# Kernel tuning notes

Hardware: AMD Instinct MI355X
Metric: run time of the kernel (lower is better)

The kernel has to match this reference:

```python
import jax, jax.numpy as jnp
import numpy as np

N_NODES = 10000
N_EDGES = 640000
D = 128  # node / edge / hidden feature dim
EPS = 1e-6


def _relu_mlp(x, params):
    # Dense+relu for all layers except the last (plain Dense)
    for w, b in params[:-1]:
        x = jax.nn.relu(x @ w + b)
    w, b = params[-1]
    return x @ w + b


def _layer_norm(x, scale, bias):
    mean = jnp.mean(x, axis=-1, keepdims=True)
    var = jnp.mean(jnp.square(x - mean), axis=-1, keepdims=True)
    return (x - mean) * jax.lax.rsqrt(var + EPS) * scale + bias


def _he(key, fan_in, fan_out):
    return jax.random.normal(key, (fan_in, fan_out), jnp.float32) * jnp.sqrt(2.0 / fan_in)


def setup_inputs() -> dict:
    key = jax.random.key(0)
    ks = jax.random.split(key, 12)
    nodes = jax.random.normal(ks[0], (N_NODES, D), jnp.float32)
    edges = jax.random.normal(ks[1], (N_EDGES, D), jnp.float32)
    senders = jax.random.randint(ks[2], (N_EDGES,), 0, N_NODES, jnp.int32)
    receivers = jax.random.randint(ks[3], (N_EDGES,), 0, N_NODES, jnp.int32)
    # MessageMLP: [3D -> D -> D -> D]
    msg_w0 = _he(ks[4], 3 * D, D); msg_b0 = jnp.zeros((D,), jnp.float32)
    msg_w1 = _he(ks[5], D, D);     msg_b1 = jnp.zeros((D,), jnp.float32)
    msg_w2 = _he(ks[6], D, D);     msg_b2 = jnp.zeros((D,), jnp.float32)
    # NodeMLP: [2D -> D -> D -> D]
    node_w0 = _he(ks[7], 2 * D, D); node_b0 = jnp.zeros((D,), jnp.float32)
    node_w1 = _he(ks[8], D, D);     node_b1 = jnp.zeros((D,), jnp.float32)
    node_w2 = _he(ks[9], D, D);     node_b2 = jnp.zeros((D,), jnp.float32)
    # W_node residual projection (no bias) + LayerNorm params
    w_node = _he(ks[10], D, D)
    ln_scale = jnp.ones((D,), jnp.float32)
    ln_bias = jnp.zeros((D,), jnp.float32)
    return dict(nodes=nodes, edges=edges, senders=senders, receivers=receivers,
                msg_w0=msg_w0, msg_b0=msg_b0, msg_w1=msg_w1, msg_b1=msg_b1,
                msg_w2=msg_w2, msg_b2=msg_b2,
                node_w0=node_w0, node_b0=node_b0, node_w1=node_w1, node_b1=node_b1,
                node_w2=node_w2, node_b2=node_b2,
                w_node=w_node, ln_scale=ln_scale, ln_bias=ln_bias)


def reference(nodes, edges, senders, receivers,
              msg_w0, msg_b0, msg_w1, msg_b1, msg_w2, msg_b2,
              node_w0, node_b0, node_w1, node_b1, node_w2, node_b2,
              w_node, ln_scale, ln_bias):
    total_nodes = nodes.shape[0]
    # gather sender/receiver features and concat with edge features: [E, 3D]
    msg_in = jnp.concatenate([nodes[senders], nodes[receivers], edges], axis=-1)
    messages = _relu_mlp(msg_in, [(msg_w0, msg_b0), (msg_w1, msg_b1), (msg_w2, msg_b2)])
    # scatter-add messages onto receiving nodes: [N, D]
    aggregated = jax.ops.segment_sum(messages, receivers, num_segments=total_nodes)
    node_in = jnp.concatenate([nodes, aggregated], axis=-1)  # [N, 2D]
    nodes_out = _relu_mlp(node_in, [(node_w0, node_b0), (node_w1, node_b1), (node_w2, node_b2)])
    nodes_new = _layer_norm(nodes @ w_node + nodes_out, ln_scale, ln_bias)
    return nodes_new
```

## Files before the change

### kernel.cpp

```cpp
#include <hip/hip_runtime.h>

#define DF 128
constexpr int N_NODES = 10000;
constexpr int N_EDGES = 640000;

typedef __bf16 bf16x8 __attribute__((ext_vector_type(8)));
typedef float f32x4 __attribute__((ext_vector_type(4)));

__device__ __forceinline__ unsigned short f2bf(float f) {
  unsigned u = __builtin_bit_cast(unsigned, f);
  u += 0x7fffu + ((u >> 16) & 1u);
  return (unsigned short)(u >> 16);
}

__device__ __forceinline__ bf16x8 cvt8(float4 a, float4 b) {
  bf16x8 r;
  r[0] = (__bf16)a.x; r[1] = (__bf16)a.y; r[2] = (__bf16)a.z; r[3] = (__bf16)a.w;
  r[4] = (__bf16)b.x; r[5] = (__bf16)b.y; r[6] = (__bf16)b.z; r[7] = (__bf16)b.w;
  return r;
}

template <bool RELU>
__device__ __forceinline__ void stage_t(char* bufj, const f32x4* accv, int grp, int row16) {
#pragma unroll
  for (int nt = 0; nt < 8; ++nt)
#pragma unroll
    for (int i = 0; i < 4; ++i) {
      const int r = grp * 4 + i;
      const int c = nt * 16 + row16;
      float v = RELU ? fmaxf(accv[nt][i], 0.f) : accv[nt][i];
      *(unsigned short*)(bufj + ((r * 256 + c * 2) ^ ((r & 7) << 4))) = f2bf(v);
    }
}

__device__ __forceinline__ bf16x8 read_a(const char* bufj, int kt, int grp, int row16) {
  return *(const bf16x8*)(bufj + ((row16 * 256 + kt * 64 + grp * 16) ^ ((row16 & 7) << 4)));
}

__global__ void pack_prep(const float* __restrict__ w0, const float* __restrict__ w1,
                          const float* __restrict__ w2, const float* __restrict__ nw0,
                          const float* __restrict__ nw1, const float* __restrict__ nw2,
                          const float* __restrict__ wn, const float* __restrict__ nodes,
                          unsigned short* __restrict__ dst, unsigned short* __restrict__ nbf) {
  int tid = blockIdx.x * blockDim.x + threadIdx.x;
  if (tid >= 163840 + N_NODES * DF) return;
  if (tid >= 163840) {
    int p = tid - 163840;
    nbf[p] = f2bf(nodes[p]);
    return;
  }
  const float* src; int p;
  if (tid < 49152)       { src = w0;  p = tid; }
  else if (tid < 65536)  { src = w1;  p = tid - 49152; }
  else if (tid < 81920)  { src = w2;  p = tid - 65536; }
  else if (tid < 114688) { src = nw0; p = tid - 81920; }
  else if (tid < 131072) { src = nw1; p = tid - 114688; }
  else if (tid < 147456) { src = nw2; p = tid - 131072; }
  else                   { src = wn;  p = tid - 147456; }
  int i = p & 7, lane = (p >> 3) & 63, tile = p >> 9;
  int nt = tile & 7, kt = tile >> 3;
  int k = kt * 32 + ((lane >> 4) << 3) + i;
  int n = nt * 16 + (lane & 15);
  dst[tid] = f2bf(src[k * 128 + n]);
}

__global__ void hist_kernel(const int* __restrict__ receivers, int* __restrict__ deg) {
  int e = blockIdx.x * blockDim.x + threadIdx.x;
  if (e < N_EDGES) atomicAdd(&deg[receivers[e]], 1);
}

__global__ void scan_kernel(const int* __restrict__ deg, int* __restrict__ rowstart) {
  __shared__ int part[1024];
  const int t = threadIdx.x;
  int loc[16];
  int s = 0;
#pragma unroll
  for (int j = 0; j < 16; ++j) {
    int idx = t * 16 + j;
    int v = (idx < N_NODES) ? deg[idx] : 0;
    loc[j] = s;
    s += v;
  }
  part[t] = s;
  __syncthreads();
  for (int off = 1; off < 1024; off <<= 1) {
    int v = part[t];
    int a = (t >= off) ? part[t - off] : 0;
    __syncthreads();
    part[t] = v + a;
    __syncthreads();
  }
  int base = (t > 0) ? part[t - 1] : 0;
#pragma unroll
  for (int j = 0; j < 16; ++j) {
    int idx = t * 16 + j;
    if (idx < N_NODES) rowstart[idx] = base + loc[j];
  }
  if (t == 0) rowstart[N_NODES] = part[1023];
}

__global__ void scatter_idx(const int* __restrict__ receivers, const int* __restrict__ senders,
                            const int* __restrict__ rowstart,
                            int* __restrict__ cursor, int* __restrict__ eid,
                            int* __restrict__ rid, int* __restrict__ ssend) {
  int e = blockIdx.x * blockDim.x + threadIdx.x;
  if (e >= N_EDGES) return;
  int r = receivers[e];
  int pos = atomicAdd(&cursor[r], 1);
  int q = rowstart[r] + pos;
  eid[q] = e;
  rid[q] = r;
  ssend[q] = senders[e];
}

__global__ void __launch_bounds__(256) pq_kernel(
    const unsigned short* __restrict__ nbf, const unsigned short* __restrict__ pw,
    float* __restrict__ P, float* __restrict__ Q) {
  const int tid = threadIdx.x, lane = tid & 63, wave = tid >> 6;
  const int row16 = lane & 15, grp = lane >> 4;
  const int rb = blockIdx.x * 64 + wave * 16;
  const int rA = min(rb + row16, N_NODES - 1);

  f32x4 aP[8], aQ[8];
#pragma unroll
  for (int nt = 0; nt < 8; ++nt) {
    aP[nt] = (f32x4){0.f, 0.f, 0.f, 0.f};
    aQ[nt] = (f32x4){0.f, 0.f, 0.f, 0.f};
  }
#pragma unroll
  for (int kt = 0; kt < 4; ++kt) {
    bf16x8 af = *(const bf16x8*)(nbf + (size_t)rA * DF + kt * 32 + grp * 8);
#pragma unroll
    for (int nt = 0; nt < 8; ++nt) {
      bf16x8 bwP = *(const bf16x8*)(pw + ((size_t)(kt * 8 + nt) * 64 + lane) * 8);
      bf16x8 bwQ = *(const bf16x8*)(pw + ((size_t)((4 + kt) * 8 + nt) * 64 + lane) * 8);
      aP[nt] = __builtin_amdgcn_mfma_f32_16x16x32_bf16(af, bwP, aP[nt], 0, 0, 0);
      aQ[nt] = __builtin_amdgcn_mfma_f32_16x16x32_bf16(af, bwQ, aQ[nt], 0, 0, 0);
    }
  }
#pragma unroll
  for (int nt = 0; nt < 8; ++nt)
#pragma unroll
    for (int i = 0; i < 4; ++i) {
      const int r = rb + grp * 4 + i;
      if (r < N_NODES) {
        P[(size_t)r * DF + nt * 16 + row16] = aP[nt][i];
        Q[(size_t)r * DF + nt * 16 + row16] = aQ[nt][i];
      }
    }
}

__global__ void __launch_bounds__(256, 2) msg_kernel(
    const float* __restrict__ edges,
    const int* __restrict__ eid, const int* __restrict__ rid, const int* __restrict__ ssend,
    const float* __restrict__ b0, const float* __restrict__ b1,
    const unsigned short* __restrict__ pw,
    const float* __restrict__ P, const float* __restrict__ Q,
    float* __restrict__ hsum) {
  __shared__ char hs[65536];
  const int tid = threadIdx.x;
  const int lane = tid & 63, wave = tid >> 6;
  const int row16 = lane & 15, grp = lane >> 4;
  char* hb = hs + wave * 16384;
  const int pbase = blockIdx.x * 256 + wave * 64;

  int e_[4], rx[4], sx[4];
#pragma unroll
  for (int s = 0; s < 4; ++s) {
    const int p = pbase + s * 16 + row16;
    e_[s] = eid[p];
    rx[s] = rid[p];
    sx[s] = ssend[p];
  }

  bf16x8 ebf[4][4];
  {
    float4 t0[4][2], t1[4][2];
#pragma unroll
    for (int k2 = 0; k2 < 4; ++k2) {
      const float* p0 = edges + (size_t)e_[0] * DF + k2 * 32 + grp * 8;
      const float* p1 = edges + (size_t)e_[1] * DF + k2 * 32 + grp * 8;
      t0[k2][0] = *(const float4*)p0; t0[k2][1] = *(const float4*)(p0 + 4);
      t1[k2][0] = *(const float4*)p1; t1[k2][1] = *(const float4*)(p1 + 4);
    }
#pragma unroll
    for (int k2 = 0; k2 < 4; ++k2) {
      ebf[0][k2] = cvt8(t0[k2][0], t0[k2][1]);
      ebf[1][k2] = cvt8(t1[k2][0], t1[k2][1]);
    }
#pragma unroll
    for (int k2 = 0; k2 < 4; ++k2) {
      const float* p2 = edges + (size_t)e_[2] * DF + k2 * 32 + grp * 8;
      const float* p3 = edges + (size_t)e_[3] * DF + k2 * 32 + grp * 8;
      t0[k2][0] = *(const float4*)p2; t0[k2][1] = *(const float4*)(p2 + 4);
      t1[k2][0] = *(const float4*)p3; t1[k2][1] = *(const float4*)(p3 + 4);
    }
#pragma unroll
    for (int k2 = 0; k2 < 4; ++k2) {
      ebf[2][k2] = cvt8(t0[k2][0], t0[k2][1]);
      ebf[3][k2] = cvt8(t1[k2][0], t1[k2][1]);
    }
  }

  f32x4 acc[4][8];
#pragma unroll
  for (int nt = 0; nt < 8; ++nt) {
    float bv = b0[nt * 16 + row16];
#pragma unroll
    for (int s = 0; s < 4; ++s) acc[s][nt] = (f32x4){bv, bv, bv, bv};
  }
#pragma unroll
  for (int kt = 0; kt < 4; ++kt) {
#pragma unroll
    for (int nt = 0; nt < 8; ++nt) {
      bf16x8 bw = *(const bf16x8*)(pw + ((size_t)((8 + kt) * 8 + nt) * 64 + lane) * 8);
#pragma unroll
      for (int s = 0; s < 4; ++s)
        acc[s][nt] = __builtin_amdgcn_mfma_f32_16x16x32_bf16(ebf[s][kt], bw, acc[s][nt], 0, 0, 0);
    }
  }

#pragma unroll
  for (int s = 0; s < 4; ++s) stage_t<false>(hb + s * 4096, acc[s], grp, row16);
  asm volatile("s_waitcnt lgkmcnt(0)" ::: "memory");
  __builtin_amdgcn_sched_barrier(0);

  f32x4 acc2[4][8];
#pragma unroll
  for (int nt = 0; nt < 8; ++nt) {
    float bv = b1[nt * 16 + row16];
#pragma unroll
    for (int s = 0; s < 4; ++s) acc2[s][nt] = (f32x4){bv, bv, bv, bv};
  }
  const unsigned short* w1p = pw + 49152;
#pragma unroll
  for (int kt = 0; kt < 4; ++kt) {
    bf16x8 af[4];
#pragma unroll
    for (int s = 0; s < 4; ++s) {
      const float* pp = P + (size_t)sx[s] * DF + kt * 32 + grp * 8;
      const float* qq = Q + (size_t)rx[s] * DF + kt * 32 + grp * 8;
      float4 p0 = *(const float4*)pp, p1 = *(const float4*)(pp + 4);
      float4 q0 = *(const float4*)qq, q1 = *(const float4*)(qq + 4);
      bf16x8 raw = read_a(hb + s * 4096, kt, grp, row16);
      bf16x8 h;
      h[0] = (__bf16)fmaxf((float)raw[0] + p0.x + q0.x, 0.f);
      h[1] = (__bf16)fmaxf((float)raw[1] + p0.y + q0.y, 0.f);
      h[2] = (__bf16)fmaxf((float)raw[2] + p0.z + q0.z, 0.f);
      h[3] = (__bf16)fmaxf((float)raw[3] + p0.w + q0.w, 0.f);
      h[4] = (__bf16)fmaxf((float)raw[4] + p1.x + q1.x, 0.f);
      h[5] = (__bf16)fmaxf((float)raw[5] + p1.y + q1.y, 0.f);
      h[6] = (__bf16)fmaxf((float)raw[6] + p1.z + q1.z, 0.f);
      h[7] = (__bf16)fmaxf((float)raw[7] + p1.w + q1.w, 0.f);
      af[s] = h;
    }
#pragma unroll
    for (int nt = 0; nt < 8; ++nt) {
      bf16x8 bw = *(const bf16x8*)(w1p + ((size_t)(kt * 8 + nt) * 64 + lane) * 8);
#pragma unroll
      for (int s = 0; s < 4; ++s)
        acc2[s][nt] = __builtin_amdgcn_mfma_f32_16x16x32_bf16(af[s], bw, acc2[s][nt], 0, 0, 0);
    }
  }

#pragma unroll
  for (int s = 0; s < 4; ++s) {
    const int q = pbase + s * 16 + grp * 4;
    const int ru = rid[pbase + s * 16];
    const bool uni = (ru == rid[pbase + s * 16 + 15]);
    if (uni) {
#pragma unroll
      for (int nt = 0; nt < 8; ++nt) {
        float t = fmaxf(acc2[s][nt][0], 0.f) + fmaxf(acc2[s][nt][1], 0.f) +
                  fmaxf(acc2[s][nt][2], 0.f) + fmaxf(acc2[s][nt][3], 0.f);
        t += __shfl_xor(t, 16);
        t += __shfl_xor(t, 32);
        if (grp == 0)
          unsafeAtomicAdd(hsum + (size_t)ru * DF + nt * 16 + row16, t);
      }
    } else {
      const int ra = rid[q], rb_ = rid[q + 1], rc = rid[q + 2], rd = rid[q + 3];
#pragma unroll
      for (int nt = 0; nt < 8; ++nt) {
        const int col = nt * 16 + row16;
        float run = fmaxf(acc2[s][nt][0], 0.f);
        if (rb_ != ra) { unsafeAtomicAdd(hsum + (size_t)ra * DF + col, run); run = 0.f; }
        run += fmaxf(acc2[s][nt][1], 0.f);
        if (rc != rb_) { unsafeAtomicAdd(hsum + (size_t)rb_ * DF + col, run); run = 0.f; }
        run += fmaxf(acc2[s][nt][2], 0.f);
        if (rd != rc) { unsafeAtomicAdd(hsum + (size_t)rc * DF + col, run); run = 0.f; }
        run += fmaxf(acc2[s][nt][3], 0.f);
        unsafeAtomicAdd(hsum + (size_t)rd * DF + col, run);
      }
    }
  }
}

__global__ void __launch_bounds__(256) node_kernel(
    const float* __restrict__ nodes, const float* __restrict__ hsum,
    const int* __restrict__ deg, const float* __restrict__ b2,
    const float* __restrict__ nb0, const float* __restrict__ nb1, const float* __restrict__ nb2,
    const unsigned short* __restrict__ pw2,
    const unsigned short* __restrict__ pnw0, const unsigned short* __restrict__ pnw1,
    const unsigned short* __restrict__ pnw2, const unsigned short* __restrict__ pwn,
    const float* __restrict__ ln_s, const float* __restrict__ ln_b,
    float* __restrict__ out) {
  __shared__ char hs[16384];
  const int tid = threadIdx.x, lane = tid & 63, wave = tid >> 6;
  const int row16 = lane & 15, grp = lane >> 4;
  char* hb = hs + wave * 4096;
  const int rb = blockIdx.x * 64 + wave * 16;
  const int rA = min(rb + row16, N_NODES - 1);

  f32x4 accA[8];
  {
    float d0 = (float)deg[min(rb + grp * 4 + 0, N_NODES - 1)];
    float d1 = (float)deg[min(rb + grp * 4 + 1, N_NODES - 1)];
    float d2 = (float)deg[min(rb + grp * 4 + 2, N_NODES - 1)];
    float d3 = (float)deg[min(rb + grp * 4 + 3, N_NODES - 1)];
#pragma unroll
    for (int nt = 0; nt < 8; ++nt) {
      float bc = b2[nt * 16 + row16];
      accA[nt] = (f32x4){d0 * bc, d1 * bc, d2 * bc, d3 * bc};
    }
  }
#pragma unroll
  for (int kt = 0; kt < 4; ++kt) {
    const float* hp = hsum + (size_t)rA * DF + kt * 32 + grp * 8;
    float4 h0 = *(const float4*)hp, h1v = *(const float4*)(hp + 4);
    bf16x8 hi = cvt8(h0, h1v);
    float4 l0, l1;
    l0.x = h0.x - (float)hi[0]; l0.y = h0.y - (float)hi[1];
    l0.z = h0.z - (float)hi[2]; l0.w = h0.w - (float)hi[3];
    l1.x = h1v.x - (float)hi[4]; l1.y = h1v.y - (float)hi[5];
    l1.z = h1v.z - (float)hi[6]; l1.w = h1v.w - (float)hi[7];
    bf16x8 lo = cvt8(l0, l1);
#pragma unroll
    for (int nt = 0; nt < 8; ++nt) {
      bf16x8 bw = *(const bf16x8*)(pw2 + ((size_t)(kt * 8 + nt) * 64 + lane) * 8);
      accA[nt] = __builtin_amdgcn_mfma_f32_16x16x32_bf16(hi, bw, accA[nt], 0, 0, 0);
      accA[nt] = __builtin_amdgcn_mfma_f32_16x16x32_bf16(lo, bw, accA[nt], 0, 0, 0);
    }
  }
  stage_t<false>(hb, accA, grp, row16);
  asm volatile("s_waitcnt lgkmcnt(0)" ::: "memory");
  __builtin_amdgcn_sched_barrier(0);

  f32x4 acc[8];
#pragma unroll
  for (int nt = 0; nt < 8; ++nt) {
    float b = nb0[nt * 16 + row16];
    acc[nt] = (f32x4){b, b, b, b};
  }
#pragma unroll
  for (int kt = 0; kt < 8; ++kt) {
    bf16x8 af;
    if (kt < 4) {
      const float* p = nodes + (size_t)rA * DF + kt * 32 + grp * 8;
      af = cvt8(*(const float4*)p, *(const float4*)(p + 4));
    } else {
      af = read_a(hb, kt - 4, grp, row16);
    }
#pragma unroll
    for (int nt = 0; nt < 8; ++nt) {
      bf16x8 bw = *(const bf16x8*)(pnw0 + ((size_t)(kt * 8 + nt) * 64 + lane) * 8);
      acc[nt] = __builtin_amdgcn_mfma_f32_16x16x32_bf16(af, bw, acc[nt], 0, 0, 0);
    }
  }
  asm volatile("s_waitcnt lgkmcnt(0)" ::: "memory");
  __builtin_amdgcn_sched_barrier(0);
  stage_t<true>(hb, acc, grp, row16);
  asm volatile("s_waitcnt lgkmcnt(0)" ::: "memory");
  __builtin_amdgcn_sched_barrier(0);

  f32x4 acc2[8];
#pragma unroll
  for (int nt = 0; nt < 8; ++nt) {
    float b = nb1[nt * 16 + row16];
    acc2[nt] = (f32x4){b, b, b, b};
  }
#pragma unroll
  for (int kt = 0; kt < 4; ++kt) {
    bf16x8 af = read_a(hb, kt, grp, row16);
#pragma unroll
    for (int nt = 0; nt < 8; ++nt) {
      bf16x8 bw = *(const bf16x8*)(pnw1 + ((size_t)(kt * 8 + nt) * 64 + lane) * 8);
      acc2[nt] = __builtin_amdgcn_mfma_f32_16x16x32_bf16(af, bw, acc2[nt], 0, 0, 0);
    }
  }
  asm volatile("s_waitcnt lgkmcnt(0)" ::: "memory");
  __builtin_amdgcn_sched_barrier(0);
  stage_t<true>(hb, acc2, grp, row16);
  asm volatile("s_waitcnt lgkmcnt(0)" ::: "memory");
  __builtin_amdgcn_sched_barrier(0);

  f32x4 acc3[8];
#pragma unroll
  for (int nt = 0; nt < 8; ++nt) {
    float b = nb2[nt * 16 + row16];
    acc3[nt] = (f32x4){b, b, b, b};
  }
#pragma unroll
  for (int kt = 0; kt < 4; ++kt) {
    bf16x8 af = read_a(hb, kt, grp, row16);
#pragma unroll
    for (int nt = 0; nt < 8; ++nt) {
      bf16x8 bw = *(const bf16x8*)(pnw2 + ((size_t)(kt * 8 + nt) * 64 + lane) * 8);
      acc3[nt] = __builtin_amdgcn_mfma_f32_16x16x32_bf16(af, bw, acc3[nt], 0, 0, 0);
    }
  }
  f32x4 accR[8];
#pragma unroll
  for (int nt = 0; nt < 8; ++nt) accR[nt] = (f32x4){0.f, 0.f, 0.f, 0.f};
#pragma unroll
  for (int kt = 0; kt < 4; ++kt) {
    const float* p = nodes + (size_t)rA * DF + kt * 32 + grp * 8;
    bf16x8 af = cvt8(*(const float4*)p, *(const float4*)(p + 4));
#pragma unroll
    for (int nt = 0; nt < 8; ++nt) {
      bf16x8 bw = *(const bf16x8*)(pwn + ((size_t)(kt * 8 + nt) * 64 + lane) * 8);
      accR[nt] = __builtin_amdgcn_mfma_f32_16x16x32_bf16(af, bw, accR[nt], 0, 0, 0);
    }
  }

  float y[8][4];
#pragma unroll
  for (int nt = 0; nt < 8; ++nt)
#pragma unroll
    for (int i = 0; i < 4; ++i) y[nt][i] = acc3[nt][i] + accR[nt][i];

  float mean[4], rstd[4];
#pragma unroll
  for (int i = 0; i < 4; ++i) {
    float s = 0.f;
#pragma unroll
    for (int nt = 0; nt < 8; ++nt) s += y[nt][i];
    s += __shfl_xor(s, 1); s += __shfl_xor(s, 2);
    s += __shfl_xor(s, 4); s += __shfl_xor(s, 8);
    mean[i] = s * (1.0f / 128.0f);
  }
#pragma unroll
  for (int i = 0; i < 4; ++i) {
    float v = 0.f;
#pragma unroll
    for (int nt = 0; nt < 8; ++nt) {
      float d = y[nt][i] - mean[i];
      v += d * d;
    }
    v += __shfl_xor(v, 1); v += __shfl_xor(v, 2);
    v += __shfl_xor(v, 4); v += __shfl_xor(v, 8);
    rstd[i] = rsqrtf(v * (1.0f / 128.0f) + 1e-6f);
  }
#pragma unroll
  for (int nt = 0; nt < 8; ++nt) {
    const float ls = ln_s[nt * 16 + row16];
    const float lb = ln_b[nt * 16 + row16];
#pragma unroll
    for (int i = 0; i < 4; ++i) {
      const int r = rb + grp * 4 + i;
      if (r < N_NODES)
        out[(size_t)r * DF + nt * 16 + row16] = (y[nt][i] - mean[i]) * rstd[i] * ls + lb;
    }
  }
}

extern "C" void kernel_launch(void* const* d_in, const int* in_sizes, int n_in,
                              void* d_out, int out_size, void* d_ws, size_t ws_size,
                              hipStream_t stream) {
  const float* nodes     = (const float*)d_in[0];
  const float* edges     = (const float*)d_in[1];
  const int*   senders   = (const int*)d_in[2];
  const int*   receivers = (const int*)d_in[3];
  const float* msg_w0 = (const float*)d_in[4];
  const float* msg_b0 = (const float*)d_in[5];
  const float* msg_w1 = (const float*)d_in[6];
  const float* msg_b1 = (const float*)d_in[7];
  const float* msg_w2 = (const float*)d_in[8];
  const float* msg_b2 = (const float*)d_in[9];
  const float* node_w0 = (const float*)d_in[10];
  const float* node_b0 = (const float*)d_in[11];
  const float* node_w1 = (const float*)d_in[12];
  const float* node_b1 = (const float*)d_in[13];
  const float* node_w2 = (const float*)d_in[14];
  const float* node_b2 = (const float*)d_in[15];
  const float* w_node   = (const float*)d_in[16];
  const float* ln_scale = (const float*)d_in[17];
  const float* ln_bias  = (const float*)d_in[18];

  char* ws = (char*)d_ws;
  float* hsum           = (float*)ws;
  unsigned short* pw    = (unsigned short*)(ws + 5120000);
  unsigned short* nbf   = (unsigned short*)(ws + 5447680);
  int* deg              = (int*)(ws + 8007680);
  int* cursor           = (int*)(ws + 8047680);
  int* rowstart         = (int*)(ws + 8087680);
  int* eid              = (int*)(ws + 8127688);
  int* rid              = (int*)(ws + 10687688);
  int* ssend            = (int*)(ws + 13247688);
  float* P              = (float*)(ws + 15807744);
  float* Q              = (float*)(ws + 20927744);

  hipMemsetAsync(hsum, 0, (size_t)N_NODES * DF * sizeof(float), stream);
  hipMemsetAsync(deg, 0, 80000, stream);

  pack_prep<<<(163840 + N_NODES * DF) / 256, 256, 0, stream>>>(
      msg_w0, msg_w1, msg_w2, node_w0, node_w1, node_w2, w_node, nodes, pw, nbf);

  hist_kernel<<<N_EDGES / 256, 256, 0, stream>>>(receivers, deg);
  scan_kernel<<<1, 1024, 0, stream>>>(deg, rowstart);
  scatter_idx<<<N_EDGES / 256, 256, 0, stream>>>(receivers, senders, rowstart, cursor,
                                                 eid, rid, ssend);
  pq_kernel<<<157, 256, 0, stream>>>(nbf, pw, P, Q);

  msg_kernel<<<N_EDGES / 256, 256, 0, stream>>>(
      edges, eid, rid, ssend, msg_b0, msg_b1, pw, P, Q, hsum);

  node_kernel<<<157, 256, 0, stream>>>(nodes, hsum, deg, msg_b2,
                                       node_b0, node_b1, node_b2,
                                       pw + 65536,
                                       pw + 81920, pw + 114688, pw + 131072, pw + 147456,
                                       ln_scale, ln_bias, (float*)d_out);
}
```

Measured before the change: 380.9 us.

## Halve per-wave edge tiles in msg kernel, fuse histogram, pack edge indices

The message kernel now handles 32 edges per wave instead of 64. It reuses one accumulator array for both layers, uses half the shared memory and raises launch bounds to 3 blocks per CU, all to raise occupancy and hide gather latency. The degree histogram is folded into pack_prep, which removes one launch. Edge id and sender are packed into an int2 for a single load. The node kernel uses 128-thread blocks, giving more blocks across CUs. In exchange, each weight fragment load now feeds fewer MFMAs, so per-MFMA weight traffic goes up.

```diff
diff --git a/kernel.cpp b/kernel.cpp
--- a/kernel.cpp
+++ b/kernel.cpp
@@ -41,32 +41,33 @@
                           const float* __restrict__ w2, const float* __restrict__ nw0,
                           const float* __restrict__ nw1, const float* __restrict__ nw2,
                           const float* __restrict__ wn, const float* __restrict__ nodes,
-                          unsigned short* __restrict__ dst, unsigned short* __restrict__ nbf) {
+                          const int* __restrict__ receivers,
+                          unsigned short* __restrict__ dst, unsigned short* __restrict__ nbf,
+                          int* __restrict__ deg) {
   int tid = blockIdx.x * blockDim.x + threadIdx.x;
-  if (tid >= 163840 + N_NODES * DF) return;
-  if (tid >= 163840) {
-    int p = tid - 163840;
+  if (tid < 163840) {
+    const float* src; int p;
+    if (tid < 49152)       { src = w0;  p = tid; }
+    else if (tid < 65536)  { src = w1;  p = tid - 49152; }
+    else if (tid < 81920)  { src = w2;  p = tid - 65536; }
+    else if (tid < 114688) { src = nw0; p = tid - 81920; }
+    else if (tid < 131072) { src = nw1; p = tid - 114688; }
+    else if (tid < 147456) { src = nw2; p = tid - 131072; }
+    else                   { src = wn;  p = tid - 147456; }
+    int i = p & 7, lane = (p >> 3) & 63, tile = p >> 9;
+    int nt = tile & 7, kt = tile >> 3;
+    int k = kt * 32 + ((lane >> 4) << 3) + i;
+    int n = nt * 16 + (lane & 15);
+    dst[tid] = f2bf(src[k * 128 + n]);
+    return;
+  }
+  int p = tid - 163840;
+  if (p < N_NODES * DF) {
     nbf[p] = f2bf(nodes[p]);
     return;
   }
-  const float* src; int p;
-  if (tid < 49152)       { src = w0;  p = tid; }
-  else if (tid < 65536)  { src = w1;  p = tid - 49152; }
-  else if (tid < 81920)  { src = w2;  p = tid - 65536; }
-  else if (tid < 114688) { src = nw0; p = tid - 81920; }
-  else if (tid < 131072) { src = nw1; p = tid - 114688; }
-  else if (tid < 147456) { src = nw2; p = tid - 131072; }
-  else                   { src = wn;  p = tid - 147456; }
-  int i = p & 7, lane = (p >> 3) & 63, tile = p >> 9;
-  int nt = tile & 7, kt = tile >> 3;
-  int k = kt * 32 + ((lane >> 4) << 3) + i;
-  int n = nt * 16 + (lane & 15);
-  dst[tid] = f2bf(src[k * 128 + n]);
-}
-
-__global__ void hist_kernel(const int* __restrict__ receivers, int* __restrict__ deg) {
-  int e = blockIdx.x * blockDim.x + threadIdx.x;
-  if (e < N_EDGES) atomicAdd(&deg[receivers[e]], 1);
+  p -= N_NODES * DF;
+  if (p < N_EDGES) atomicAdd(&deg[receivers[p]], 1);
 }
 
 __global__ void scan_kernel(const int* __restrict__ deg, int* __restrict__ rowstart) {
@@ -101,16 +102,15 @@
 
 __global__ void scatter_idx(const int* __restrict__ receivers, const int* __restrict__ senders,
                             const int* __restrict__ rowstart,
-                            int* __restrict__ cursor, int* __restrict__ eid,
-                            int* __restrict__ rid, int* __restrict__ ssend) {
+                            int* __restrict__ cursor, int2* __restrict__ ep,
+                            int* __restrict__ rid) {
   int e = blockIdx.x * blockDim.x + threadIdx.x;
   if (e >= N_EDGES) return;
   int r = receivers[e];
   int pos = atomicAdd(&cursor[r], 1);
   int q = rowstart[r] + pos;
-  eid[q] = e;
+  ep[q] = make_int2(e, senders[e]);
   rid[q] = r;
-  ssend[q] = senders[e];
 }
 
 __global__ void __launch_bounds__(256) pq_kernel(
@@ -150,30 +150,30 @@
     }
 }
 
-__global__ void __launch_bounds__(256, 2) msg_kernel(
+__global__ void __launch_bounds__(256, 3) msg_kernel(
     const float* __restrict__ edges,
-    const int* __restrict__ eid, const int* __restrict__ rid, const int* __restrict__ ssend,
+    const int2* __restrict__ ep, const int* __restrict__ rid,
     const float* __restrict__ b0, const float* __restrict__ b1,
     const unsigned short* __restrict__ pw,
     const float* __restrict__ P, const float* __restrict__ Q,
     float* __restrict__ hsum) {
-  __shared__ char hs[65536];
+  __shared__ char hs[32768];
   const int tid = threadIdx.x;
   const int lane = tid & 63, wave = tid >> 6;
   const int row16 = lane & 15, grp = lane >> 4;
-  char* hb = hs + wave * 16384;
-  const int pbase = blockIdx.x * 256 + wave * 64;
-
-  int e_[4], rx[4], sx[4];
-#pragma unroll
-  for (int s = 0; s < 4; ++s) {
-    const int p = pbase + s * 16 + row16;
-    e_[s] = eid[p];
-    rx[s] = rid[p];
-    sx[s] = ssend[p];
-  }
-
-  bf16x8 ebf[4][4];
+  char* hb = hs + wave * 8192;
+  const int pbase = blockIdx.x * 128 + wave * 32;
+
+  int e_[2], sx[2], rx[2];
+#pragma unroll
+  for (int s = 0; s < 2; ++s) {
+    int2 es = ep[pbase + s * 16 + row16];
+    e_[s] = es.x;
+    sx[s] = es.y;
+    rx[s] = rid[pbase + s * 16 + row16];
+  }
+
+  bf16x8 ebf[2][4];
   {
     float4 t0[4][2], t1[4][2];
 #pragma unroll
@@ -188,56 +188,42 @@
       ebf[0][k2] = cvt8(t0[k2][0], t0[k2][1]);
       ebf[1][k2] = cvt8(t1[k2][0], t1[k2][1]);
     }
-#pragma unroll
-    for (int k2 = 0; k2 < 4; ++k2) {
-      const float* p2 = edges + (size_t)e_[2] * DF + k2 * 32 + grp * 8;
-      const float* p3 = edges + (size_t)e_[3] * DF + k2 * 32 + grp * 8;
-      t0[k2][0] = *(const float4*)p2; t0[k2][1] = *(const float4*)(p2 + 4);
-      t1[k2][0] = *(const float4*)p3; t1[k2][1] = *(const float4*)(p3 + 4);
-    }
-#pragma unroll
-    for (int k2 = 0; k2 < 4; ++k2) {
-      ebf[2][k2] = cvt8(t0[k2][0], t0[k2][1]);
-      ebf[3][k2] = cvt8(t1[k2][0], t1[k2][1]);
-    }
-  }
-
-  f32x4 acc[4][8];
+  }
+
+  f32x4 acc[2][8];
 #pragma unroll
   for (int nt = 0; nt < 8; ++nt) {
     float bv = b0[nt * 16 + row16];
-#pragma unroll
-    for (int s = 0; s < 4; ++s) acc[s][nt] = (f32x4){bv, bv, bv, bv};
+    acc[0][nt] = (f32x4){bv, bv, bv, bv};
+    acc[1][nt] = (f32x4){bv, bv, bv, bv};
   }
 #pragma unroll
   for (int kt = 0; kt < 4; ++kt) {
 #pragma unroll
     for (int nt = 0; nt < 8; ++nt) {
       bf16x8 bw = *(const bf16x8*)(pw + ((size_t)((8 + kt) * 8 + nt) * 64 + lane) * 8);
-#pragma unroll
-      for (int s = 0; s < 4; ++s)
-        acc[s][nt] = __builtin_amdgcn_mfma_f32_16x16x32_bf16(ebf[s][kt], bw, acc[s][nt], 0, 0, 0);
-    }
-  }
-
-#pragma unroll
-  for (int s = 0; s < 4; ++s) stage_t<false>(hb + s * 4096, acc[s], grp, row16);
+      acc[0][nt] = __builtin_amdgcn_mfma_f32_16x16x32_bf16(ebf[0][kt], bw, acc[0][nt], 0, 0, 0);
+      acc[1][nt] = __builtin_amdgcn_mfma_f32_16x16x32_bf16(ebf[1][kt], bw, acc[1][nt], 0, 0, 0);
+    }
+  }
+
+  stage_t<false>(hb, acc[0], grp, row16);
+  stage_t<false>(hb + 4096, acc[1], grp, row16);
   asm volatile("s_waitcnt lgkmcnt(0)" ::: "memory");
   __builtin_amdgcn_sched_barrier(0);
 
-  f32x4 acc2[4][8];
 #pragma unroll
   for (int nt = 0; nt < 8; ++nt) {
     float bv = b1[nt * 16 + row16];
-#pragma unroll
-    for (int s = 0; s < 4; ++s) acc2[s][nt] = (f32x4){bv, bv, bv, bv};
+    acc[0][nt] = (f32x4){bv, bv, bv, bv};
+    acc[1][nt] = (f32x4){bv, bv, bv, bv};
   }
   const unsigned short* w1p = pw + 49152;
 #pragma unroll
   for (int kt = 0; kt < 4; ++kt) {
-    bf16x8 af[4];
-#pragma unroll
-    for (int s = 0; s < 4; ++s) {
+    bf16x8 af[2];
+#pragma unroll
+    for (int s = 0; s < 2; ++s) {
       const float* pp = P + (size_t)sx[s] * DF + kt * 32 + grp * 8;
       const float* qq = Q + (size_t)rx[s] * DF + kt * 32 + grp * 8;
       float4 p0 = *(const float4*)pp, p1 = *(const float4*)(pp + 4);
@@ -257,22 +243,21 @@
 #pragma unroll
     for (int nt = 0; nt < 8; ++nt) {
       bf16x8 bw = *(const bf16x8*)(w1p + ((size_t)(kt * 8 + nt) * 64 + lane) * 8);
-#pragma unroll
-      for (int s = 0; s < 4; ++s)
-        acc2[s][nt] = __builtin_amdgcn_mfma_f32_16x16x32_bf16(af[s], bw, acc2[s][nt], 0, 0, 0);
-    }
-  }
-
-#pragma unroll
-  for (int s = 0; s < 4; ++s) {
+      acc[0][nt] = __builtin_amdgcn_mfma_f32_16x16x32_bf16(af[0], bw, acc[0][nt], 0, 0, 0);
+      acc[1][nt] = __builtin_amdgcn_mfma_f32_16x16x32_bf16(af[1], bw, acc[1][nt], 0, 0, 0);
+    }
+  }
+
+#pragma unroll
+  for (int s = 0; s < 2; ++s) {
     const int q = pbase + s * 16 + grp * 4;
     const int ru = rid[pbase + s * 16];
     const bool uni = (ru == rid[pbase + s * 16 + 15]);
     if (uni) {
 #pragma unroll
       for (int nt = 0; nt < 8; ++nt) {
-        float t = fmaxf(acc2[s][nt][0], 0.f) + fmaxf(acc2[s][nt][1], 0.f) +
-                  fmaxf(acc2[s][nt][2], 0.f) + fmaxf(acc2[s][nt][3], 0.f);
+        float t = fmaxf(acc[s][nt][0], 0.f) + fmaxf(acc[s][nt][1], 0.f) +
+                  fmaxf(acc[s][nt][2], 0.f) + fmaxf(acc[s][nt][3], 0.f);
         t += __shfl_xor(t, 16);
         t += __shfl_xor(t, 32);
         if (grp == 0)
@@ -283,20 +268,20 @@
 #pragma unroll
       for (int nt = 0; nt < 8; ++nt) {
         const int col = nt * 16 + row16;
-        float run = fmaxf(acc2[s][nt][0], 0.f);
+        float run = fmaxf(acc[s][nt][0], 0.f);
         if (rb_ != ra) { unsafeAtomicAdd(hsum + (size_t)ra * DF + col, run); run = 0.f; }
-        run += fmaxf(acc2[s][nt][1], 0.f);
+        run += fmaxf(acc[s][nt][1], 0.f);
         if (rc != rb_) { unsafeAtomicAdd(hsum + (size_t)rb_ * DF + col, run); run = 0.f; }
-        run += fmaxf(acc2[s][nt][2], 0.f);
+        run += fmaxf(acc[s][nt][2], 0.f);
         if (rd != rc) { unsafeAtomicAdd(hsum + (size_t)rc * DF + col, run); run = 0.f; }
-        run += fmaxf(acc2[s][nt][3], 0.f);
+        run += fmaxf(acc[s][nt][3], 0.f);
         unsafeAtomicAdd(hsum + (size_t)rd * DF + col, run);
       }
     }
   }
 }
 
-__global__ void __launch_bounds__(256) node_kernel(
+__global__ void __launch_bounds__(128) node_kernel(
     const float* __restrict__ nodes, const float* __restrict__ hsum,
     const int* __restrict__ deg, const float* __restrict__ b2,
     const float* __restrict__ nb0, const float* __restrict__ nb1, const float* __restrict__ nb2,
@@ -305,11 +290,11 @@
     const unsigned short* __restrict__ pnw2, const unsigned short* __restrict__ pwn,
     const float* __restrict__ ln_s, const float* __restrict__ ln_b,
     float* __restrict__ out) {
-  __shared__ char hs[16384];
+  __shared__ char hs[8192];
   const int tid = threadIdx.x, lane = tid & 63, wave = tid >> 6;
   const int row16 = lane & 15, grp = lane >> 4;
   char* hb = hs + wave * 4096;
-  const int rb = blockIdx.x * 64 + wave * 16;
+  const int rb = blockIdx.x * 32 + wave * 16;
   const int rA = min(rb + row16, N_NODES - 1);
 
   f32x4 accA[8];
@@ -494,28 +479,27 @@
   int* deg              = (int*)(ws + 8007680);
   int* cursor           = (int*)(ws + 8047680);
   int* rowstart         = (int*)(ws + 8087680);
-  int* eid              = (int*)(ws + 8127688);
-  int* rid              = (int*)(ws + 10687688);
-  int* ssend            = (int*)(ws + 13247688);
-  float* P              = (float*)(ws + 15807744);
-  float* Q              = (float*)(ws + 20927744);
+  int* rid              = (int*)(ws + 8127688);
+  int2* ep              = (int2*)(ws + 10687688);
+  float* P              = (float*)(ws + 15807696);
+  float* Q              = (float*)(ws + 20927696);
 
   hipMemsetAsync(hsum, 0, (size_t)N_NODES * DF * sizeof(float), stream);
   hipMemsetAsync(deg, 0, 80000, stream);
 
-  pack_prep<<<(163840 + N_NODES * DF) / 256, 256, 0, stream>>>(
-      msg_w0, msg_w1, msg_w2, node_w0, node_w1, node_w2, w_node, nodes, pw, nbf);
-
-  hist_kernel<<<N_EDGES / 256, 256, 0, stream>>>(receivers, deg);
+  pack_prep<<<8140, 256, 0, stream>>>(
+      msg_w0, msg_w1, msg_w2, node_w0, node_w1, node_w2, w_node, nodes, receivers,
+      pw, nbf, deg);
+
   scan_kernel<<<1, 1024, 0, stream>>>(deg, rowstart);
   scatter_idx<<<N_EDGES / 256, 256, 0, stream>>>(receivers, senders, rowstart, cursor,
-                                                 eid, rid, ssend);
+                                                 ep, rid);
   pq_kernel<<<157, 256, 0, stream>>>(nbf, pw, P, Q);
 
-  msg_kernel<<<N_EDGES / 256, 256, 0, stream>>>(
-      edges, eid, rid, ssend, msg_b0, msg_b1, pw, P, Q, hsum);
-
-  node_kernel<<<157, 256, 0, stream>>>(nodes, hsum, deg, msg_b2,
+  msg_kernel<<<N_EDGES / 128, 256, 0, stream>>>(
+      edges, ep, rid, msg_b0, msg_b1, pw, P, Q, hsum);
+
+  node_kernel<<<313, 128, 0, stream>>>(nodes, hsum, deg, msg_b2,
                                        node_b0, node_b1, node_b2,
                                        pw + 65536,
                                        pw + 81920, pw + 114688, pw + 131072, pw + 147456,
```

New measurement: 420.6 us. 1.1x slower.
